# Kernel optimization log

Measured on AMD Instinct MI355X. Metric: run time of the kernel, lower is better.

Reference implementation:

```python
import jax, jax.numpy as jnp
import numpy as np

SAMPLE_RATE = 48000.0
WIN_SIZE = 512   # also the FFT size (nfft = win_size in forward)
HOP_SIZE = 256   # win_size // 2, COLA with Hann
B = 128
NUM_FREQ_PTS = 96000  # 2 s RIR at 48 kHz


def _hann(n):
    # torch.hann_window default is periodic: 0.5*(1 - cos(2*pi*k/n))
    k = jnp.arange(n, dtype=jnp.float32)
    return 0.5 * (1.0 - jnp.cos(2.0 * jnp.pi * k / n))


def _stft(x, win, nfft, hop):
    # x: [B, L] real. center=False, onesided=True, not normalized.
    L = x.shape[-1]
    pad = (-L) % hop  # pad to multiple of hop, as in get_stft_torch
    if pad:
        x = jnp.pad(x, ((0, 0), (0, pad)))
    T = (x.shape[-1] - nfft) // hop + 1  # number of frames
    idx = hop * jnp.arange(T)[:, None] + jnp.arange(nfft)[None, :]  # [T, nfft]
    frames = x[:, idx] * win  # [B, T, nfft]
    return jnp.fft.rfft(frames, n=nfft, axis=-1)  # [B, T, F], F = nfft//2 + 1


def _edr_db(S):
    # S: [B, T, F] complex. EDR[m] = sum_{t>=m} |S[t]|^2  -> reverse cumsum (O(T)).
    P = jnp.abs(S) ** 2  # [B, T, F]
    edr = jnp.flip(jnp.cumsum(jnp.flip(P, axis=1), axis=1), axis=1)
    return 10.0 * jnp.log10(edr)  # db(..., is_squared=True)


def reference(target_re, target_im, ach_re, ach_im):
    n = target_re.shape[-1]
    target_rir = jnp.fft.irfft(target_re + 1j * target_im, n=n)
    ach_rir = jnp.fft.irfft(ach_re + 1j * ach_im, n=n)
    win = _hann(WIN_SIZE)
    S_t = _stft(target_rir, win, WIN_SIZE, HOP_SIZE)
    S_a = _stft(ach_rir, win, WIN_SIZE, HOP_SIZE)
    edr_t = _edr_db(S_t)
    edr_a = _edr_db(S_a)
    return jnp.sum(jnp.abs(edr_t - edr_a)) / jnp.sum(jnp.abs(edr_t))


def setup_inputs() -> dict:
    key = jax.random.key(0)
    k1, k2, k3, k4 = jax.random.split(key, 4)
    shape = (B, NUM_FREQ_PTS)
    return {
        "target_re": jax.random.normal(k1, shape, dtype=jnp.float32),
        "target_im": jax.random.normal(k2, shape, dtype=jnp.float32),
        "ach_re": jax.random.normal(k3, shape, dtype=jnp.float32),
        "ach_im": jax.random.normal(k4, shape, dtype=jnp.float32),
    }
```

## Files before the change

kernel.cpp:

```cpp
#include <hip/hip_runtime.h>
#include <math.h>

#define BATCH   128
#define NFREQ   96000
#define M_HALF  48000
#define NFRAMES 374
#define NBINS   257
#define NG      11
#define GLEN    34
#define FPW     4

#define CS1 246
#define CS2 206

#define PI_D 3.14159265358979323846

#define WAVE_SYNC() __asm__ volatile("s_waitcnt lgkmcnt(0)" ::: "memory")

__device__ __forceinline__ float2 cmulf(float2 a, float2 b) {
  return make_float2(a.x * b.x - a.y * b.y, a.x * b.y + a.y * b.x);
}

__device__ __forceinline__ void bfly4(float2 z0, float2 z1, float2 z2, float2 z3,
                                      float2& o0, float2& o1, float2& o2, float2& o3) {
  float2 e0 = make_float2(z0.x + z2.x, z0.y + z2.y);
  float2 e1 = make_float2(z0.x - z2.x, z0.y - z2.y);
  float2 e2 = make_float2(z1.x + z3.x, z1.y + z3.y);
  float2 e3 = make_float2(z1.x - z3.x, z1.y - z3.y);
  o0 = make_float2(e0.x + e2.x, e0.y + e2.y);
  o2 = make_float2(e0.x - e2.x, e0.y - e2.y);
  o1 = make_float2(e1.x + e3.y, e1.y - e3.x);
  o3 = make_float2(e1.x - e3.y, e1.y + e3.x);
}

__device__ __forceinline__ void bfly4i(float2 z0, float2 z1, float2 z2, float2 z3,
                                       float2& o0, float2& o1, float2& o2, float2& o3) {
  float2 e0 = make_float2(z0.x + z2.x, z0.y + z2.y);
  float2 e1 = make_float2(z0.x - z2.x, z0.y - z2.y);
  float2 e2 = make_float2(z1.x + z3.x, z1.y + z3.y);
  float2 e3 = make_float2(z1.x - z3.x, z1.y - z3.y);
  o0 = make_float2(e0.x + e2.x, e0.y + e2.y);
  o2 = make_float2(e0.x - e2.x, e0.y - e2.y);
  o1 = make_float2(e1.x - e3.y, e1.y + e3.x);
  o3 = make_float2(e1.x + e3.y, e1.y - e3.x);
}

#define PIDX(i) ((i) + ((i) >> 3))

__global__ void setup_kernel(float2* __restrict__ Wm, float2* __restrict__ Wpack,
                             float2* __restrict__ W512, float* __restrict__ hann,
                             float2* __restrict__ W240, float2* __restrict__ W200,
                             float2* __restrict__ Wp240) {
  int i = blockIdx.x * blockDim.x + threadIdx.x;
  if (i < M_HALF) {
    double th = 2.0 * PI_D * (double)i / (double)M_HALF;
    double s, c; sincos(th, &s, &c);
    Wm[i] = make_float2((float)c, (float)s);
    double th2 = PI_D * (double)i / (double)M_HALF;
    double s2, c2; sincos(th2, &s2, &c2);
    Wpack[i] = make_float2((float)c2, (float)s2);
  }
  if (i < 512) {
    double th = -2.0 * PI_D * (double)i / 512.0;
    double s, c; sincos(th, &s, &c);
    W512[i] = make_float2((float)c, (float)s);
    hann[i] = (float)(0.5 * (1.0 - cos(2.0 * PI_D * (double)i / 512.0)));
  }
  if (i < 240) {
    double th = 2.0 * PI_D * (double)i / 240.0;
    double s, c; sincos(th, &s, &c);
    W240[i] = make_float2((float)c, (float)s);
    double th2 = PI_D * (double)i / 240.0;
    double s2, c2; sincos(th2, &s2, &c2);
    Wp240[i] = make_float2((float)c2, (float)s2);
  }
  if (i < 200) {
    double th = 2.0 * PI_D * (double)i / 200.0;
    double s, c; sincos(th, &s, &c);
    W200[i] = make_float2((float)c, (float)s);
  }
}

__global__ __launch_bounds__(256) void k1_kernel(
    const float* __restrict__ tre, const float* __restrict__ tim,
    const float* __restrict__ are, const float* __restrict__ aim,
    float2* __restrict__ G, const float2* __restrict__ Wm,
    const float2* __restrict__ Wpack, const float2* __restrict__ Wp240,
    const float2* __restrict__ W240, int b0, int c) {
  __shared__ float2 LA[8 * CS1];
  __shared__ float2 LB[8 * CS1];
  const int tid = threadIdx.x;
  const int row = blockIdx.y;
  const int K0 = blockIdx.x * 8;

  const int isA = row >= c;
  const int b = b0 + (isA ? row - c : row);
  const float* rr = (isA ? are : tre) + (size_t)b * NFREQ;
  const float* ii = (isA ? aim : tim) + (size_t)b * NFREQ;

  {
    const int k1o = tid & 7;
    const float2 wpa = Wpack[K0 + k1o];
    const float sc = 1.0f / (float)M_HALF;
    for (int e = tid; e < 8 * 240; e += 256) {
      int k2 = e >> 3;
      int k = K0 + k1o + 200 * k2;
      float xr = rr[k];
      float xi = (k == 0) ? 0.f : ii[k];
      int mk = M_HALF - k;
      float yr = rr[mk];
      float yi = (k == 0) ? 0.f : ii[mk];
      float Er = 0.5f * (xr + yr);
      float Ei = 0.5f * (xi - yi);
      float Dr = 0.5f * (xr - yr);
      float Di = 0.5f * (xi + yi);
      float2 wp = cmulf(wpa, Wp240[k2]);
      float tr = wp.x * Dr - wp.y * Di;
      float ti = wp.x * Di + wp.y * Dr;
      LA[k1o * CS1 + k2] = make_float2((Er - ti) * sc, (Ei + tr) * sc);
    }
  }
  __syncthreads();
  for (int e = tid; e < 8 * 60; e += 256) {
    int col = e & 7, p = e >> 3;
    const float2* in = LA + col * CS1;
    float2 o0, o1, o2, o3;
    bfly4i(in[p], in[p + 60], in[p + 120], in[p + 180], o0, o1, o2, o3);
    o1 = cmulf(o1, W240[p]);
    o2 = cmulf(o2, W240[2 * p]);
    o3 = cmulf(o3, W240[3 * p]);
    float2* out = LB + col * CS1 + 4 * p;
    out[0] = o0; out[1] = o1; out[2] = o2; out[3] = o3;
  }
  __syncthreads();
  for (int e = tid; e < 8 * 60; e += 256) {
    int col = e & 7, t = e >> 3;
    int q = t & 3, p = t >> 2;
    const float2* in = LB + col * CS1;
    float2 o0, o1, o2, o3;
    bfly4i(in[q + 4 * p], in[q + 4 * (p + 15)], in[q + 4 * (p + 30)],
           in[q + 4 * (p + 45)], o0, o1, o2, o3);
    o1 = cmulf(o1, W240[4 * p]);
    o2 = cmulf(o2, W240[8 * p]);
    o3 = cmulf(o3, W240[12 * p]);
    float2* out = LA + col * CS1 + q;
    out[4 * (4 * p + 0)] = o0; out[4 * (4 * p + 1)] = o1;
    out[4 * (4 * p + 2)] = o2; out[4 * (4 * p + 3)] = o3;
  }
  __syncthreads();
  {
    float2 w15[15];
#pragma unroll
    for (int m = 0; m < 15; ++m) w15[m] = W240[16 * m];
    for (int e = tid; e < 8 * 16; e += 256) {
      int col = e & 7, q = e >> 3;
      const float2* in = LA + col * CS1 + q;
      float2 a[15];
#pragma unroll
      for (int j = 0; j < 15; ++j) a[j] = in[16 * j];
      float2* out = LB + col * CS1 + q;
#pragma unroll
      for (int u = 0; u < 15; ++u) {
        float2 acc = a[0];
#pragma unroll
        for (int j = 1; j < 15; ++j) {
          float2 w = w15[(u * j) % 15];
          acc.x += a[j].x * w.x - a[j].y * w.y;
          acc.y += a[j].x * w.y + a[j].y * w.x;
        }
        out[16 * u] = acc;
      }
    }
  }
  __syncthreads();
  {
    const int col = tid & 7;
    const int k1 = K0 + col;
    int n2 = tid >> 3;
    float2 tw = Wm[k1 * n2];
    const float2 twstep = Wm[32 * k1];
    float2* Grow = G + (size_t)row * M_HALF;
    const float2* in = LB + col * CS1;
    for (; n2 < 240; n2 += 32) {
      Grow[(size_t)n2 * 200 + k1] = cmulf(in[n2], tw);
      tw = cmulf(tw, twstep);
    }
  }
}

__global__ __launch_bounds__(256) void k2_kernel(
    const float2* __restrict__ G, float2* __restrict__ X,
    const float2* __restrict__ W200) {
  __shared__ float2 LA[8 * CS2];
  __shared__ float2 LB[8 * CS2];
  const int tid = threadIdx.x;
  const int row = blockIdx.y;
  const int N20 = blockIdx.x * 8;
  const float2* Grow = G + (size_t)row * M_HALF;

  for (int e = tid; e < 8 * 200; e += 256) {
    int n2o = e / 200;
    int k1 = e - n2o * 200;
    LA[n2o * CS2 + k1] = Grow[(size_t)(N20 + n2o) * 200 + k1];
  }
  __syncthreads();
  for (int e = tid; e < 8 * 50; e += 256) {
    int col = e & 7, p = e >> 3;
    const float2* in = LA + col * CS2;
    float2 o0, o1, o2, o3;
    bfly4i(in[p], in[p + 50], in[p + 100], in[p + 150], o0, o1, o2, o3);
    o1 = cmulf(o1, W200[p]);
    o2 = cmulf(o2, W200[2 * p]);
    o3 = cmulf(o3, W200[3 * p]);
    float2* out = LB + col * CS2 + 4 * p;
    out[0] = o0; out[1] = o1; out[2] = o2; out[3] = o3;
  }
  __syncthreads();
  {
    float2 w5[5];
#pragma unroll
    for (int m = 0; m < 5; ++m) w5[m] = W200[40 * m];
    for (int e = tid; e < 8 * 40; e += 256) {
      int col = e & 7, t = e >> 3;
      int q = t & 3, p = t >> 2;
      const float2* in = LB + col * CS2 + q;
      float2 a[5];
#pragma unroll
      for (int j = 0; j < 5; ++j) a[j] = in[4 * (p + 10 * j)];
      float2* out = LA + col * CS2 + q;
#pragma unroll
      for (int u = 0; u < 5; ++u) {
        float2 acc = a[0];
#pragma unroll
        for (int j = 1; j < 5; ++j) {
          float2 w = w5[(u * j) % 5];
          acc.x += a[j].x * w.x - a[j].y * w.y;
          acc.y += a[j].x * w.y + a[j].y * w.x;
        }
        acc = cmulf(acc, W200[4 * u * p]);
        out[4 * (5 * p + u)] = acc;
      }
    }
  }
  __syncthreads();
  {
    float2 w10[10];
#pragma unroll
    for (int m = 0; m < 10; ++m) w10[m] = W200[20 * m];
    for (int e = tid; e < 8 * 20; e += 256) {
      int col = e & 7, q = e >> 3;
      const float2* in = LA + col * CS2 + q;
      float2 a[10];
#pragma unroll
      for (int j = 0; j < 10; ++j) a[j] = in[20 * j];
      float2* out = LB + col * CS2 + q;
#pragma unroll
      for (int u = 0; u < 10; ++u) {
        float2 acc = a[0];
#pragma unroll
        for (int j = 1; j < 10; ++j) {
          float2 w = w10[(u * j) % 10];
          acc.x += a[j].x * w.x - a[j].y * w.y;
          acc.y += a[j].x * w.y + a[j].y * w.x;
        }
        out[20 * u] = acc;
      }
    }
  }
  __syncthreads();
  {
    const int n2o = tid & 7;
    float2* Xrow = X + (size_t)row * M_HALF + (N20 + n2o);
    const float2* in = LB + n2o * CS2;
    for (int n1 = tid >> 3; n1 < 200; n1 += 32)
      Xrow[240 * n1] = in[n1];
  }
}

__global__ __launch_bounds__(256) void stft256_kernel(
    const float* __restrict__ xtime, float* __restrict__ P,
    const float2* __restrict__ W512, const float* __restrict__ hann) {
  __shared__ float2 lds[4][2][288];
  const int tid = threadIdx.x;
  const int wave = tid >> 6;
  const int l = tid & 63;
  const int row = blockIdx.y;
  const int frame0 = (blockIdx.x * 4 + wave) * FPW;

  float2* Abuf = lds[wave][0];
  float2* Bbuf = lds[wave][1];

  const float2* hann2 = (const float2*)hann;
  float2 hw[4];
#pragma unroll
  for (int j = 0; j < 4; ++j) hw[j] = hann2[l + 64 * j];
  float2 t1[3], t2[3], t3[3];
  {
    int p2 = l >> 2, p3 = l >> 4;
#pragma unroll
    for (int u = 1; u <= 3; ++u) {
      t1[u - 1] = W512[2 * u * l];
      t2[u - 1] = W512[8 * u * p2];
      t3[u - 1] = W512[32 * u * p3];
    }
  }

  const float2* xrow = (const float2*)xtime + (size_t)row * 48000;

  for (int fi = 0; fi < FPW; ++fi) {
    const int fr = frame0 + fi;
    const bool active = (fr < NFRAMES);
    float2 z[4];
    if (active) {
      const float2* src = xrow + fr * 128;
#pragma unroll
      for (int j = 0; j < 4; ++j) {
        float2 v = src[l + 64 * j];
        z[j] = make_float2(v.x * hw[j].x, v.y * hw[j].y);
      }
    } else {
#pragma unroll
      for (int j = 0; j < 4; ++j) z[j] = make_float2(0.f, 0.f);
    }
    float2 o0, o1, o2, o3;
    bfly4(z[0], z[1], z[2], z[3], o0, o1, o2, o3);
    o1 = cmulf(o1, t1[0]); o2 = cmulf(o2, t1[1]); o3 = cmulf(o3, t1[2]);
    Abuf[PIDX(4 * l + 0)] = o0; Abuf[PIDX(4 * l + 1)] = o1;
    Abuf[PIDX(4 * l + 2)] = o2; Abuf[PIDX(4 * l + 3)] = o3;
    WAVE_SYNC();
    {
      int q = l & 3, p = l >> 2;
      float2 a0 = Abuf[PIDX(q + 4 * p)];
      float2 a1 = Abuf[PIDX(q + 4 * (p + 16))];
      float2 a2 = Abuf[PIDX(q + 4 * (p + 32))];
      float2 a3 = Abuf[PIDX(q + 4 * (p + 48))];
      bfly4(a0, a1, a2, a3, o0, o1, o2, o3);
      o1 = cmulf(o1, t2[0]); o2 = cmulf(o2, t2[1]); o3 = cmulf(o3, t2[2]);
      int wb = q + 16 * p;
      Bbuf[PIDX(wb)] = o0; Bbuf[PIDX(wb + 4)] = o1;
      Bbuf[PIDX(wb + 8)] = o2; Bbuf[PIDX(wb + 12)] = o3;
    }
    WAVE_SYNC();
    {
      int q = l & 15, p = l >> 4;
      float2 a0 = Bbuf[PIDX(q + 16 * p)];
      float2 a1 = Bbuf[PIDX(q + 16 * (p + 4))];
      float2 a2 = Bbuf[PIDX(q + 16 * (p + 8))];
      float2 a3 = Bbuf[PIDX(q + 16 * (p + 12))];
      bfly4(a0, a1, a2, a3, o0, o1, o2, o3);
      o1 = cmulf(o1, t3[0]); o2 = cmulf(o2, t3[1]); o3 = cmulf(o3, t3[2]);
      int wb = q + 64 * p;
      Abuf[PIDX(wb)] = o0; Abuf[PIDX(wb + 16)] = o1;
      Abuf[PIDX(wb + 32)] = o2; Abuf[PIDX(wb + 48)] = o3;
    }
    WAVE_SYNC();
    {
      float2 a0 = Abuf[PIDX(l)];
      float2 a1 = Abuf[PIDX(l + 64)];
      float2 a2 = Abuf[PIDX(l + 128)];
      float2 a3 = Abuf[PIDX(l + 192)];
      bfly4(a0, a1, a2, a3, o0, o1, o2, o3);
      Bbuf[PIDX(l)] = o0; Bbuf[PIDX(l + 64)] = o1;
      Bbuf[PIDX(l + 128)] = o2; Bbuf[PIDX(l + 192)] = o3;
    }
    WAVE_SYNC();
    if (active) {
      float* Prow = P + ((size_t)row * NFRAMES + fr) * NBINS;
      for (int k = l; k <= 256; k += 64) {
        float2 Zk = Bbuf[PIDX(k & 255)];
        float2 Zm = Bbuf[PIDX((256 - k) & 255)];
        float2 E  = make_float2(0.5f * (Zk.x + Zm.x), 0.5f * (Zk.y - Zm.y));
        float2 Op = make_float2(Zk.x - Zm.x, Zk.y + Zm.y);
        float2 Od = make_float2(0.5f * Op.y, -0.5f * Op.x);
        float2 W  = W512[k];
        float2 Xb = make_float2(E.x + W.x * Od.x - W.y * Od.y,
                                E.y + W.x * Od.y + W.y * Od.x);
        Prow[k] = Xb.x * Xb.x + Xb.y * Xb.y;
      }
    }
    WAVE_SYNC();
  }
}

__global__ __launch_bounds__(256) void edrA_kernel(const float* __restrict__ P,
                                                   float* __restrict__ part) {
  const int r = blockIdx.x;
  const int g = blockIdx.y;
  const float* Pr = P + (size_t)r * (NFRAMES * NBINS);
  for (int bin = threadIdx.x; bin < NBINS; bin += 256) {
    float s = 0.f;
    const int m0 = g * GLEN;
    for (int m = m0; m < m0 + GLEN; ++m) s += Pr[m * NBINS + bin];
    part[((size_t)r * NG + g) * NBINS + bin] = s;
  }
}

__global__ __launch_bounds__(256) void edrB_kernel(const float* __restrict__ P,
                                                   const float* __restrict__ part,
                                                   double* __restrict__ accum, int c) {
  const int b = blockIdx.x;
  const int g = blockIdx.y;
  const float* Pt = P + (size_t)b * (NFRAMES * NBINS);
  const float* Pa = P + (size_t)(b + c) * (NFRAMES * NBINS);
  const float* qt = part + (size_t)b * NG * NBINS;
  const float* qa = part + (size_t)(b + c) * NG * NBINS;
  float sn = 0.f, sd = 0.f;
  for (int bin = threadIdx.x; bin < NBINS; bin += 256) {
    float ct = 0.f, ca = 0.f;
    for (int g2 = g + 1; g2 < NG; ++g2) {
      ct += qt[g2 * NBINS + bin];
      ca += qa[g2 * NBINS + bin];
    }
    const int m0 = g * GLEN;
    for (int m = m0 + GLEN - 1; m >= m0; --m) {
      ct += Pt[m * NBINS + bin];
      ca += Pa[m * NBINS + bin];
      float lt = 10.f * log10f(ct);
      float la = 10.f * log10f(ca);
      sn += fabsf(lt - la);
      sd += fabsf(lt);
    }
  }
#pragma unroll
  for (int off = 32; off > 0; off >>= 1) {
    sn += __shfl_down(sn, off, 64);
    sd += __shfl_down(sd, off, 64);
  }
  __shared__ float wsn[4], wsd[4];
  const int wave = threadIdx.x >> 6;
  if ((threadIdx.x & 63) == 0) { wsn[wave] = sn; wsd[wave] = sd; }
  __syncthreads();
  if (threadIdx.x == 0) {
    float tn = 0.f, td = 0.f;
#pragma unroll
    for (int w = 0; w < 4; ++w) { tn += wsn[w]; td += wsd[w]; }
    int slot = (blockIdx.x * NG + blockIdx.y) & 63;
    atomicAdd(&accum[slot], (double)tn);
    atomicAdd(&accum[64 + slot], (double)td);
  }
}

__global__ void final_kernel(const double* __restrict__ accum, float* __restrict__ out) {
  double n = 0.0, d = 0.0;
  for (int i = 0; i < 64; ++i) { n += accum[i]; d += accum[64 + i]; }
  out[0] = (float)(n / d);
}

extern "C" void kernel_launch(void* const* d_in, const int* in_sizes, int n_in,
                              void* d_out, int out_size, void* d_ws, size_t ws_size,
                              hipStream_t stream) {
  const float* tre = (const float*)d_in[0];
  const float* tim = (const float*)d_in[1];
  const float* are = (const float*)d_in[2];
  const float* aim = (const float*)d_in[3];
  float* out = (float*)d_out;

  char* base = (char*)d_ws;
  size_t off = 0;
  auto take = [&](size_t bytes) -> char* {
    char* p = base + off;
    off += (bytes + 255) & ~(size_t)255;
    return p;
  };
  float2* Wm    = (float2*)take((size_t)M_HALF * sizeof(float2));
  float2* Wpack = (float2*)take((size_t)M_HALF * sizeof(float2));
  float2* W512  = (float2*)take(512 * sizeof(float2));
  float*  hann  = (float*)take(512 * sizeof(float));
  float2* W240  = (float2*)take(240 * sizeof(float2));
  float2* W200  = (float2*)take(200 * sizeof(float2));
  float2* Wp240 = (float2*)take(240 * sizeof(float2));
  double* accum = (double*)take(128 * sizeof(double));
  size_t fixed = off;

  const size_t perA    = (size_t)2 * M_HALF * sizeof(float2);
  const size_t perP    = (size_t)2 * NFRAMES * NBINS * sizeof(float);
  const size_t perPart = (size_t)2 * NG * NBINS * sizeof(float);
  int c = 1;
  const int cands[8] = {128, 64, 32, 16, 8, 4, 2, 1};
  for (int ci = 0; ci < 8; ++ci) {
    size_t need = fixed + ((cands[ci] * perA + 255) & ~(size_t)255)
                        + ((cands[ci] * perP + 255) & ~(size_t)255)
                        + ((cands[ci] * perPart + 255) & ~(size_t)255);
    if (need <= ws_size) { c = cands[ci]; break; }
  }
  float2* Z    = (float2*)take((size_t)c * perA);
  char*   BP   = take((size_t)c * perP);
  float*  part = (float*)take((size_t)c * perPart);
  float2* G = (float2*)BP;
  float*  P = (float*)BP;

  setup_kernel<<<(M_HALF + 255) / 256, 256, 0, stream>>>(Wm, Wpack, W512, hann,
                                                         W240, W200, Wp240);
  hipMemsetAsync(accum, 0, 128 * sizeof(double), stream);

  for (int b0 = 0; b0 < BATCH; b0 += c) {
    int rows = 2 * c;
    k1_kernel<<<dim3(25, rows), 256, 0, stream>>>(tre, tim, are, aim, G, Wm,
                                                  Wpack, Wp240, W240, b0, c);
    k2_kernel<<<dim3(30, rows), 256, 0, stream>>>(G, Z, W200);
    {
      dim3 grid((NFRAMES + 4 * FPW - 1) / (4 * FPW), rows);
      stft256_kernel<<<grid, 256, 0, stream>>>((const float*)Z, P, W512, hann);
    }
    edrA_kernel<<<dim3(rows, NG), 256, 0, stream>>>(P, part);
    edrB_kernel<<<dim3(c, NG), 256, 0, stream>>>(P, part, accum, c);
  }
  final_kernel<<<1, 1, 0, stream>>>(accum, out);
}
```

Baseline: 451.9 us.

## Split real-FFT packing into coalesced transpose kernel before first FFT stage

The irfft pre-packing step (even/odd split with mirrored indices and twiddle multiply) moves out of k1 into a new packT kernel. packT reads contiguous input chunks into shared memory and writes a transposed packed array, so k1 can load its columns contiguously instead of with the strided gathers it used before. This targets uncoalesced global reads in k1, at the cost of an extra kernel launch and an extra full write and read of the packed intermediate. The buffer is reused for k2's output.

After: 448.0 us. Within noise of the previous version (-0.9%).

```diff
diff --git a/kernel.cpp b/kernel.cpp
--- a/kernel.cpp
+++ b/kernel.cpp
@@ -49,8 +49,7 @@
 
 __global__ void setup_kernel(float2* __restrict__ Wm, float2* __restrict__ Wpack,
                              float2* __restrict__ W512, float* __restrict__ hann,
-                             float2* __restrict__ W240, float2* __restrict__ W200,
-                             float2* __restrict__ Wp240) {
+                             float2* __restrict__ W240, float2* __restrict__ W200) {
   int i = blockIdx.x * blockDim.x + threadIdx.x;
   if (i < M_HALF) {
     double th = 2.0 * PI_D * (double)i / (double)M_HALF;
@@ -70,9 +69,6 @@
     double th = 2.0 * PI_D * (double)i / 240.0;
     double s, c; sincos(th, &s, &c);
     W240[i] = make_float2((float)c, (float)s);
-    double th2 = PI_D * (double)i / 240.0;
-    double s2, c2; sincos(th2, &s2, &c2);
-    Wp240[i] = make_float2((float)c2, (float)s2);
   }
   if (i < 200) {
     double th = 2.0 * PI_D * (double)i / 200.0;
@@ -81,43 +77,61 @@
   }
 }
 
-__global__ __launch_bounds__(256) void k1_kernel(
+__global__ __launch_bounds__(256) void packT_kernel(
     const float* __restrict__ tre, const float* __restrict__ tim,
     const float* __restrict__ are, const float* __restrict__ aim,
-    float2* __restrict__ G, const float2* __restrict__ Wm,
-    const float2* __restrict__ Wpack, const float2* __restrict__ Wp240,
-    const float2* __restrict__ W240, int b0, int c) {
+    float2* __restrict__ Zt, const float2* __restrict__ Wpack, int b0, int c) {
+  __shared__ float dRe[1600], dIm[1600], mRe[1600], mIm[1600];
+  const int tid = threadIdx.x;
+  const int row = blockIdx.y;
+  const int base = blockIdx.x * 1600;
+  const int isA = row >= c;
+  const int b = b0 + (isA ? row - c : row);
+  const float* rr = (isA ? are : tre) + (size_t)b * NFREQ;
+  const float* ii = (isA ? aim : tim) + (size_t)b * NFREQ;
+  for (int j = tid; j < 1600; j += 256) {
+    dRe[j] = rr[base + j];
+    dIm[j] = ii[base + j];
+    int mk = M_HALF - base - j;
+    mRe[j] = rr[mk];
+    mIm[j] = ii[mk];
+  }
+  __syncthreads();
+  const float sc = 1.0f / (float)M_HALF;
+  float2* Zrow = Zt + (size_t)row * M_HALF;
+  const int k2base = blockIdx.x * 8;
+  for (int e = tid; e < 1600; e += 256) {
+    int k1 = e >> 3, k2o = e & 7;
+    int j = k1 + 200 * k2o;
+    int k = base + j;
+    float xr = dRe[j], xi = dIm[j];
+    float yr = mRe[j], yi = mIm[j];
+    if (k == 0) { xi = 0.f; yi = 0.f; }
+    float Er = 0.5f * (xr + yr);
+    float Ei = 0.5f * (xi - yi);
+    float Dr = 0.5f * (xr - yr);
+    float Di = 0.5f * (xi + yi);
+    float2 wp = Wpack[k];
+    float tr = wp.x * Dr - wp.y * Di;
+    float ti = wp.x * Di + wp.y * Dr;
+    Zrow[k1 * 240 + k2base + k2o] = make_float2((Er - ti) * sc, (Ei + tr) * sc);
+  }
+}
+
+__global__ __launch_bounds__(256) void k1_kernel(
+    const float2* __restrict__ Zt, float2* __restrict__ G,
+    const float2* __restrict__ Wm, const float2* __restrict__ W240) {
   __shared__ float2 LA[8 * CS1];
   __shared__ float2 LB[8 * CS1];
   const int tid = threadIdx.x;
   const int row = blockIdx.y;
   const int K0 = blockIdx.x * 8;
 
-  const int isA = row >= c;
-  const int b = b0 + (isA ? row - c : row);
-  const float* rr = (isA ? are : tre) + (size_t)b * NFREQ;
-  const float* ii = (isA ? aim : tim) + (size_t)b * NFREQ;
-
-  {
-    const int k1o = tid & 7;
-    const float2 wpa = Wpack[K0 + k1o];
-    const float sc = 1.0f / (float)M_HALF;
-    for (int e = tid; e < 8 * 240; e += 256) {
-      int k2 = e >> 3;
-      int k = K0 + k1o + 200 * k2;
-      float xr = rr[k];
-      float xi = (k == 0) ? 0.f : ii[k];
-      int mk = M_HALF - k;
-      float yr = rr[mk];
-      float yi = (k == 0) ? 0.f : ii[mk];
-      float Er = 0.5f * (xr + yr);
-      float Ei = 0.5f * (xi - yi);
-      float Dr = 0.5f * (xr - yr);
-      float Di = 0.5f * (xi + yi);
-      float2 wp = cmulf(wpa, Wp240[k2]);
-      float tr = wp.x * Dr - wp.y * Di;
-      float ti = wp.x * Di + wp.y * Dr;
-      LA[k1o * CS1 + k2] = make_float2((Er - ti) * sc, (Ei + tr) * sc);
+  {
+    const float2* Zrow = Zt + (size_t)row * M_HALF + (size_t)K0 * 240;
+    for (int j = tid; j < 8 * 240; j += 256) {
+      int col = j / 240, k2 = j - col * 240;
+      LA[col * CS1 + k2] = Zrow[j];
     }
   }
   __syncthreads();
@@ -468,7 +482,6 @@
   float*  hann  = (float*)take(512 * sizeof(float));
   float2* W240  = (float2*)take(240 * sizeof(float2));
   float2* W200  = (float2*)take(200 * sizeof(float2));
-  float2* Wp240 = (float2*)take(240 * sizeof(float2));
   double* accum = (double*)take(128 * sizeof(double));
   size_t fixed = off;
 
@@ -483,24 +496,27 @@
                         + ((cands[ci] * perPart + 255) & ~(size_t)255);
     if (need <= ws_size) { c = cands[ci]; break; }
   }
-  float2* Z    = (float2*)take((size_t)c * perA);
+  float2* buf1 = (float2*)take((size_t)c * perA);
   char*   BP   = take((size_t)c * perP);
   float*  part = (float*)take((size_t)c * perPart);
-  float2* G = (float2*)BP;
-  float*  P = (float*)BP;
+  float2* Zt = buf1;
+  float2* X  = buf1;
+  float2* G  = (float2*)BP;
+  float*  P  = (float*)BP;
 
   setup_kernel<<<(M_HALF + 255) / 256, 256, 0, stream>>>(Wm, Wpack, W512, hann,
-                                                         W240, W200, Wp240);
+                                                         W240, W200);
   hipMemsetAsync(accum, 0, 128 * sizeof(double), stream);
 
   for (int b0 = 0; b0 < BATCH; b0 += c) {
     int rows = 2 * c;
-    k1_kernel<<<dim3(25, rows), 256, 0, stream>>>(tre, tim, are, aim, G, Wm,
-                                                  Wpack, Wp240, W240, b0, c);
-    k2_kernel<<<dim3(30, rows), 256, 0, stream>>>(G, Z, W200);
+    packT_kernel<<<dim3(30, rows), 256, 0, stream>>>(tre, tim, are, aim, Zt,
+                                                     Wpack, b0, c);
+    k1_kernel<<<dim3(25, rows), 256, 0, stream>>>(Zt, G, Wm, W240);
+    k2_kernel<<<dim3(30, rows), 256, 0, stream>>>(G, X, W200);
     {
       dim3 grid((NFRAMES + 4 * FPW - 1) / (4 * FPW), rows);
-      stft256_kernel<<<grid, 256, 0, stream>>>((const float*)Z, P, W512, hann);
+      stft256_kernel<<<grid, 256, 0, stream>>>((const float*)X, P, W512, hann);
     }
     edrA_kernel<<<dim3(rows, NG), 256, 0, stream>>>(P, part);
     edrB_kernel<<<dim3(c, NG), 256, 0, stream>>>(P, part, accum, c);
```
